# Optimization experiments

Hardware: AMD Instinct MI355X
Metric: run time of the kernel (lower is better)

## Reference

```python
import jax, jax.numpy as jnp
import numpy as np

B, L, H, F, K, NBINS, T = 32, 512, 512, 512, 3, 256, 4096
EPS = 1e-8  # RMSNorm epsilon
PAD = (K - 1) // 2  # =1, matches both conv paddings in the torch module


def _conv1d(x, w, b):
    # x: [B, L, Cin], w: [K, Cin, Cout]
    return jax.lax.conv_general_dilated(
        x, w, window_strides=(1,), padding=[(PAD, PAD)],
        dimension_numbers=('NLC', 'LIO', 'NLC')) + b


def _rms(x, g):
    return g * x / (jnp.sqrt(jnp.mean(x * x, axis=-1, keepdims=True)) + EPS)


def _vpred(x, mask, w1, b1, g1, w2, b2, g2, wl, bl):
    h = _rms(jax.nn.relu(_conv1d(x, w1, b1)), g1)
    h = _rms(jax.nn.relu(_conv1d(h, w2, b2)), g2)
    out = (h @ wl + bl)[..., 0]  # [B, L]
    return jnp.where(mask, 0.0, out)


def _proj(x, w1, b1, w2, b2):
    return jax.nn.relu(jax.nn.relu(x @ w1 + b1) @ w2 + b2)


def _length_regulate(x, dur, max_len):
    # Vectorized equivalent of LengthRegulator: repeat phoneme i dur[b,i] times, pad to max_len.
    cum = jnp.cumsum(dur, axis=1)               # [B, L]
    mel_len = cum[:, -1]                        # [B]
    t = jnp.arange(max_len)                     # [T]
    idx = jax.vmap(lambda c: jnp.searchsorted(c, t, side='right'))(cum)  # [B, T]
    idx = jnp.minimum(idx, x.shape[1] - 1)
    out = jnp.take_along_axis(x, idx[:, :, None], axis=1)  # [B, T, H]
    valid = (t[None, :] < mel_len[:, None])
    return out * valid[:, :, None].astype(x.dtype), mel_len


def setup_inputs() -> dict:
    key = jax.random.key(0)
    ks = iter(jax.random.split(key, 64))
    n = lambda *s: jax.random.normal(next(ks), s, jnp.float32) * 0.05
    inp = {}
    inp['x'] = jax.random.normal(next(ks), (B, L, H), jnp.float32)
    inp['embedding'] = jax.random.normal(next(ks), (B, L, H), jnp.float32)
    inp['src_mask'] = jnp.zeros((B, L), bool)
    inp['duration_target'] = jax.random.randint(next(ks), (B, L), 0, 9, jnp.int32)
    inp['pitch_target'] = jax.random.normal(next(ks), (B, L), jnp.float32)
    inp['energy_target'] = jax.random.normal(next(ks), (B, L), jnp.float32)
    inp['max_len'] = T
    for p in ['dur', 'pit', 'eng']:
        inp[p + '_w1'] = n(K, H, F); inp[p + '_b1'] = jnp.zeros(F, jnp.float32)
        inp[p + '_g1'] = jnp.ones(F, jnp.float32)
        inp[p + '_w2'] = n(K, F, F); inp[p + '_b2'] = jnp.zeros(F, jnp.float32)
        inp[p + '_g2'] = jnp.ones(F, jnp.float32)
        inp[p + '_wl'] = n(F, 1); inp[p + '_bl'] = jnp.zeros(1, jnp.float32)
    for p in ['pp', 'ep', 'sp']:
        inp[p + '_w1'] = n(H, H); inp[p + '_b1'] = jnp.zeros(H, jnp.float32)
        inp[p + '_w2'] = n(H, H); inp[p + '_b2'] = jnp.zeros(H, jnp.float32)
    inp['pitch_bins'] = jnp.linspace(-3.0, 3.0, NBINS - 1)
    inp['energy_bins'] = jnp.linspace(-3.0, 3.0, NBINS - 1)
    inp['pitch_emb'] = n(NBINS, H)
    inp['energy_emb'] = n(NBINS, H)
    return inp


def reference(x, embedding, src_mask, duration_target, pitch_target, energy_target, max_len,
              dur_w1, dur_b1, dur_g1, dur_w2, dur_b2, dur_g2, dur_wl, dur_bl,
              pit_w1, pit_b1, pit_g1, pit_w2, pit_b2, pit_g2, pit_wl, pit_bl,
              eng_w1, eng_b1, eng_g1, eng_w2, eng_b2, eng_g2, eng_wl, eng_bl,
              pp_w1, pp_b1, pp_w2, pp_b2,
              ep_w1, ep_b1, ep_w2, ep_b2,
              sp_w1, sp_b1, sp_w2, sp_b2,
              pitch_bins, energy_bins, pitch_emb, energy_emb):
    log_dur = _vpred(x, src_mask, dur_w1, dur_b1, dur_g1, dur_w2, dur_b2, dur_g2, dur_wl, dur_bl)
    pit_pred = _vpred(x + _proj(embedding, pp_w1, pp_b1, pp_w2, pp_b2), src_mask,
                      pit_w1, pit_b1, pit_g1, pit_w2, pit_b2, pit_g2, pit_wl, pit_bl)
    pitch_embedding = pitch_emb[jnp.searchsorted(pitch_bins, pitch_target)]  # torch.bucketize right=False == side='left'
    eng_pred = _vpred(x + _proj(embedding, ep_w1, ep_b1, ep_w2, ep_b2), src_mask,
                      eng_w1, eng_b1, eng_g1, eng_w2, eng_b2, eng_g2, eng_wl, eng_bl)
    energy_embedding = energy_emb[jnp.searchsorted(energy_bins, energy_target)]
    xo = x + energy_embedding + pitch_embedding + _proj(embedding, sp_w1, sp_b1, sp_w2, sp_b2)
    out, mel_len = _length_regulate(xo, duration_target, max_len)
    return (out, pit_pred, eng_pred, log_dur, mel_len)
```

## Files before the change

### kernel.cpp

```cpp
#include <hip/hip_runtime.h>

#define Bv    32
#define Lv    512
#define Hv    512
#define Fv    512
#define Tv    4096
#define Mv    (Bv*Lv)
#define NBINSv 256

#define OUT_OFF 0
#define PIT_OFF (Bv*(size_t)Tv*Hv)
#define ENG_OFF (PIT_OFF + Mv)
#define DUR_OFF (ENG_OFF + Mv)
#define MEL_OFF (DUR_OFF + Mv)

typedef unsigned short ushort;
typedef __attribute__((ext_vector_type(8))) short   bf16x8;
typedef __attribute__((ext_vector_type(4))) float   f32x4;
typedef __attribute__((ext_vector_type(8))) unsigned short u16x8;

__device__ __forceinline__ float b2f(ushort u) {
    union { float f; unsigned u; } x; x.u = ((unsigned)u) << 16; return x.f;
}
__device__ __forceinline__ ushort f2b(float f) {
    union { float f; unsigned u; } x; x.f = f;
    unsigned r = x.u + 0x7fffu + ((x.u >> 16) & 1u);
    return (ushort)(r >> 16);
}

#define GLL16(g, l) __builtin_amdgcn_global_load_lds( \
    (const __attribute__((address_space(1))) void*)(g), \
    (__attribute__((address_space(3))) void*)(l), 16, 0, 0)

template<int NTAPS, int EPI>
__global__ __launch_bounds__(256) void gemm_bf16_kernel(
    const ushort* __restrict__ A, const ushort* __restrict__ Bt,
    const float* __restrict__ bias, ushort* __restrict__ C,
    const float* __restrict__ res, const float* __restrict__ pe,
    const float* __restrict__ ee, const int* __restrict__ idxp,
    const int* __restrict__ idxe, const ushort* __restrict__ zp)
{
    constexpr int KTOT = NTAPS * 512;
    __shared__ ushort As[128 * 32];
    __shared__ ushort Bs[128 * 32];

    const int tid = threadIdx.x;
    const int n0 = blockIdx.x * 128;
    const int m0 = blockIdx.y * 128;

    const int sar = tid >> 2;
    const int sl  = tid & 3;

    const int lane = tid & 63;
    const int w    = tid >> 6;
    const int wm   = (w & 1) * 64;
    const int wn   = (w >> 1) * 64;
    const int lr   = lane & 15;
    const int q    = lane >> 4;

    f32x4 acc[4][4];
    #pragma unroll
    for (int i = 0; i < 4; ++i)
        #pragma unroll
        for (int j = 0; j < 4; ++j) {
            f32x4 z = {0.f, 0.f, 0.f, 0.f};
            acc[i][j] = z;
        }

    for (int kt = 0; kt < NTAPS * 16; ++kt) {
        const int tap = (NTAPS == 3) ? (kt >> 4) : 0;
        const int kin = (NTAPS == 3) ? ((kt & 15) << 5) : (kt << 5);

        #pragma unroll
        for (int r = 0; r < 2; ++r) {
            const int row = sar + r * 64;
            const int m   = m0 + row;
            const int qg  = (sl - (row >> 1)) & 3;
            const ushort* asrc;
            if (NTAPS == 3) {
                const int l  = m & (Lv - 1);
                const int ls = l + tap - 1;
                asrc = ((unsigned)ls < (unsigned)Lv)
                     ? A + (size_t)(m + tap - 1) * 512 + kin + qg * 8
                     : zp;
            } else {
                asrc = A + (size_t)m * 512 + kin + qg * 8;
            }
            GLL16(asrc, &As[row * 32 + sl * 8]);
            const ushort* bsrc = Bt + (size_t)(n0 + row) * KTOT + tap * 512 + kin + qg * 8;
            GLL16(bsrc, &Bs[row * 32 + sl * 8]);
        }
        __syncthreads();

        bf16x8 af[4], bf[4];
        #pragma unroll
        for (int i = 0; i < 4; ++i) {
            const int rm = wm + i * 16 + lr;
            af[i] = *(const bf16x8*)&As[rm * 32 + (((q + (rm >> 1)) & 3) << 3)];
            const int rn = wn + i * 16 + lr;
            bf[i] = *(const bf16x8*)&Bs[rn * 32 + (((q + (rn >> 1)) & 3) << 3)];
        }
        #pragma unroll
        for (int i = 0; i < 4; ++i)
            #pragma unroll
            for (int j = 0; j < 4; ++j)
                acc[i][j] = __builtin_amdgcn_mfma_f32_16x16x32_bf16(
                                af[i], bf[j], acc[i][j], 0, 0, 0);
        __syncthreads();
    }

    #pragma unroll
    for (int i = 0; i < 4; ++i) {
        #pragma unroll
        for (int r = 0; r < 4; ++r) {
            const int m = m0 + wm + i * 16 + q * 4 + r;
            const size_t ro = (size_t)m * 512;
            int ip = 0, ie = 0;
            if (EPI == 2) { ip = idxp[m]; ie = idxe[m]; }
            #pragma unroll
            for (int j = 0; j < 4; ++j) {
                const int n = n0 + wn + j * 16 + lr;
                float v = acc[i][j][r] + bias[n];
                v = fmaxf(v, 0.f);
                if (EPI >= 1) v += res[ro + n];
                if (EPI == 2) v += pe[(size_t)ip * 512 + n] + ee[(size_t)ie * 512 + n];
                C[ro + n] = f2b(v);
            }
        }
    }
}

__global__ __launch_bounds__(256) void convert_kernel(
    const float* __restrict__ X, ushort* __restrict__ Xb)
{
    const size_t i = (size_t)blockIdx.x * 256 + threadIdx.x;
    const float4 a = ((const float4*)X)[2 * i];
    const float4 b = ((const float4*)X)[2 * i + 1];
    u16x8 o;
    o[0] = f2b(a.x); o[1] = f2b(a.y); o[2] = f2b(a.z); o[3] = f2b(a.w);
    o[4] = f2b(b.x); o[5] = f2b(b.y); o[6] = f2b(b.z); o[7] = f2b(b.w);
    *(u16x8*)(Xb + i * 8) = o;
}

__global__ __launch_bounds__(256) void transpose_kernel(
    const float* __restrict__ W, ushort* __restrict__ Wt, int Ktot)
{
    __shared__ float t[32][33];
    const int k0 = blockIdx.x * 32, n0 = blockIdx.y * 32;
    const int r = threadIdx.x >> 5, c = threadIdx.x & 31;
    #pragma unroll
    for (int rr = 0; rr < 4; ++rr)
        t[r + rr * 8][c] = W[(size_t)(k0 + r + rr * 8) * 512 + n0 + c];
    __syncthreads();
    #pragma unroll
    for (int rr = 0; rr < 4; ++rr)
        Wt[(size_t)(n0 + r + rr * 8) * Ktot + k0 + c] = f2b(t[c][r + rr * 8]);
}

__global__ __launch_bounds__(128) void rms_kernel(
    const ushort* __restrict__ h, const float* __restrict__ g, ushort* __restrict__ o)
{
    const int row = blockIdx.x;
    const int tid = threadIdx.x;
    const ushort4 hv = ((const ushort4*)(h + (size_t)row * 512))[tid];
    const float v0 = b2f(hv.x), v1 = b2f(hv.y), v2 = b2f(hv.z), v3 = b2f(hv.w);
    float ss = v0 * v0 + v1 * v1 + v2 * v2 + v3 * v3;
    #pragma unroll
    for (int off = 32; off; off >>= 1) ss += __shfl_down(ss, off, 64);
    __shared__ float p[2];
    if ((tid & 63) == 0) p[tid >> 6] = ss;
    __syncthreads();
    const float tot = p[0] + p[1];
    const float inv = 1.f / (sqrtf(tot * (1.f / 512.f)) + 1e-8f);
    const float4 gv = ((const float4*)g)[tid];
    ushort4 ov;
    ov.x = f2b(gv.x * v0 * inv); ov.y = f2b(gv.y * v1 * inv);
    ov.z = f2b(gv.z * v2 * inv); ov.w = f2b(gv.w * v3 * inv);
    ((ushort4*)(o + (size_t)row * 512))[tid] = ov;
}

__global__ __launch_bounds__(256) void linear_kernel(
    const ushort* __restrict__ h, const float* __restrict__ wl,
    const float* __restrict__ bl, const unsigned char* __restrict__ mask,
    float* __restrict__ o)
{
    const int wave = threadIdx.x >> 6, lane = threadIdx.x & 63;
    const int row = blockIdx.x * 4 + wave;
    const bf16x8 hv = *(const bf16x8*)(h + (size_t)row * 512 + lane * 8);
    float s = 0.f;
    #pragma unroll
    for (int t = 0; t < 8; ++t) s += b2f((ushort)hv[t]) * wl[lane * 8 + t];
    #pragma unroll
    for (int off = 32; off; off >>= 1) s += __shfl_down(s, off, 64);
    if (lane == 0) o[row] = mask[row] ? 0.f : (s + bl[0]);
}

__global__ __launch_bounds__(256) void idx_kernel(
    const float* __restrict__ pt, const float* __restrict__ et,
    const float* __restrict__ pbins, const float* __restrict__ ebins,
    int* __restrict__ idxp, int* __restrict__ idxe)
{
    __shared__ float pb[NBINSv - 1], eb[NBINSv - 1];
    const int tid = threadIdx.x;
    if (tid < NBINSv - 1) { pb[tid] = pbins[tid]; eb[tid] = ebins[tid]; }
    __syncthreads();
    const int m = blockIdx.x * 256 + tid;
    const float pv = pt[m], ev = et[m];
    int lo = 0, hi = NBINSv - 1;
    while (lo < hi) { int mid = (lo + hi) >> 1; if (pb[mid] < pv) lo = mid + 1; else hi = mid; }
    idxp[m] = lo;
    lo = 0; hi = NBINSv - 1;
    while (lo < hi) { int mid = (lo + hi) >> 1; if (eb[mid] < ev) lo = mid + 1; else hi = mid; }
    idxe[m] = lo;
}

__global__ __launch_bounds__(512) void cumsum_kernel(
    const int* __restrict__ dur, int* __restrict__ cum,
    int* __restrict__ melint, float* __restrict__ melout)
{
    __shared__ int s[Lv];
    const int b = blockIdx.x, tid = threadIdx.x;
    s[tid] = dur[b * Lv + tid];
    __syncthreads();
    for (int off = 1; off < Lv; off <<= 1) {
        int t = (tid >= off) ? s[tid - off] : 0;
        __syncthreads();
        s[tid] += t;
        __syncthreads();
    }
    cum[b * Lv + tid] = s[tid];
    if (tid == Lv - 1) { melint[b] = s[tid]; melout[b] = (float)s[tid]; }
}

__global__ __launch_bounds__(128) void regulate_kernel(
    const ushort* __restrict__ xo, const int* __restrict__ cum,
    const int* __restrict__ melint, float* __restrict__ out)
{
    const int bt = blockIdx.x;
    const int b = bt >> 12;
    const int t = bt & (Tv - 1);
    const int* c = cum + b * Lv;
    int lo = 0, hi = Lv;
    while (lo < hi) { int mid = (lo + hi) >> 1; if (c[mid] <= t) lo = mid + 1; else hi = mid; }
    const int idx = min(lo, Lv - 1);
    float4 v = make_float4(0.f, 0.f, 0.f, 0.f);
    if (t < melint[b]) {
        const ushort4 u = ((const ushort4*)(xo + (size_t)(b * Lv + idx) * 512))[threadIdx.x];
        v.x = b2f(u.x); v.y = b2f(u.y); v.z = b2f(u.z); v.w = b2f(u.w);
    }
    ((float4*)(out + (size_t)bt * 512))[threadIdx.x] = v;
}

extern "C" void kernel_launch(void* const* d_in, const int* in_sizes, int n_in,
                              void* d_out, int out_size, void* d_ws, size_t ws_size,
                              hipStream_t stream)
{
    const float* x    = (const float*)d_in[0];
    const float* emb  = (const float*)d_in[1];
    const unsigned char* mask = (const unsigned char*)d_in[2];
    const int*   durt = (const int*)d_in[3];
    const float* pt   = (const float*)d_in[4];
    const float* et   = (const float*)d_in[5];
    const float* dw1 = (const float*)d_in[7],  *db1 = (const float*)d_in[8],
               * dg1 = (const float*)d_in[9],  *dw2 = (const float*)d_in[10],
               * db2 = (const float*)d_in[11], *dg2 = (const float*)d_in[12],
               * dwl = (const float*)d_in[13], *dbl = (const float*)d_in[14];
    const float* pw1 = (const float*)d_in[15], *pb1 = (const float*)d_in[16],
               * pg1 = (const float*)d_in[17], *pw2 = (const float*)d_in[18],
               * pb2 = (const float*)d_in[19], *pg2 = (const float*)d_in[20],
               * pwl = (const float*)d_in[21], *pbl = (const float*)d_in[22];
    const float* ew1 = (const float*)d_in[23], *eb1 = (const float*)d_in[24],
               * eg1 = (const float*)d_in[25], *ew2 = (const float*)d_in[26],
               * eb2 = (const float*)d_in[27], *eg2 = (const float*)d_in[28],
               * ewl = (const float*)d_in[29], *ebl = (const float*)d_in[30];
    const float* ppw1 = (const float*)d_in[31], *ppb1 = (const float*)d_in[32],
               * ppw2 = (const float*)d_in[33], *ppb2 = (const float*)d_in[34];
    const float* epw1 = (const float*)d_in[35], *epb1 = (const float*)d_in[36],
               * epw2 = (const float*)d_in[37], *epb2 = (const float*)d_in[38];
    const float* spw1 = (const float*)d_in[39], *spb1 = (const float*)d_in[40],
               * spw2 = (const float*)d_in[41], *spb2 = (const float*)d_in[42];
    const float* pbins = (const float*)d_in[43];
    const float* ebins = (const float*)d_in[44];
    const float* pemb  = (const float*)d_in[45];
    const float* eemb  = (const float*)d_in[46];

    float* outf = (float*)d_out;

    int*    cum    = (int*)d_ws;
    int*    melint = cum + Mv;
    int*    idxp   = melint + 64;
    int*    idxe   = idxp + Mv;
    ushort* zp     = (ushort*)((float*)d_ws + 49216);
    ushort* xob    = (ushort*)((float*)d_ws + 65536);

    ushort* xb   = (ushort*)(outf + 0);
    ushort* eb   = (ushort*)(outf + 4194304);
    ushort* bufA = (ushort*)(outf + 8388608);
    ushort* bufC = (ushort*)(outf + 12582912);
    ushort* bufD = (ushort*)(outf + 16777216);
    ushort* wt[12];
    {
        size_t off = 20971520;
        for (int i = 0; i < 6; ++i) { wt[i] = (ushort*)(outf + off); off += 393216; }
        for (int i = 6; i < 12; ++i) { wt[i] = (ushort*)(outf + off); off += 131072; }
    }

    hipMemsetAsync(zp, 0, 64, stream);

    convert_kernel<<<4096, 256, 0, stream>>>(x, xb);
    convert_kernel<<<4096, 256, 0, stream>>>(emb, eb);
    const dim3 tg3(48, 16), tg1(16, 16);
    transpose_kernel<<<tg3, 256, 0, stream>>>(dw1, wt[0], 1536);
    transpose_kernel<<<tg3, 256, 0, stream>>>(dw2, wt[1], 1536);
    transpose_kernel<<<tg3, 256, 0, stream>>>(pw1, wt[2], 1536);
    transpose_kernel<<<tg3, 256, 0, stream>>>(pw2, wt[3], 1536);
    transpose_kernel<<<tg3, 256, 0, stream>>>(ew1, wt[4], 1536);
    transpose_kernel<<<tg3, 256, 0, stream>>>(ew2, wt[5], 1536);
    transpose_kernel<<<tg1, 256, 0, stream>>>(ppw1, wt[6],  512);
    transpose_kernel<<<tg1, 256, 0, stream>>>(ppw2, wt[7],  512);
    transpose_kernel<<<tg1, 256, 0, stream>>>(epw1, wt[8],  512);
    transpose_kernel<<<tg1, 256, 0, stream>>>(epw2, wt[9],  512);
    transpose_kernel<<<tg1, 256, 0, stream>>>(spw1, wt[10], 512);
    transpose_kernel<<<tg1, 256, 0, stream>>>(spw2, wt[11], 512);

    idx_kernel<<<Mv / 256, 256, 0, stream>>>(pt, et, pbins, ebins, idxp, idxe);
    cumsum_kernel<<<Bv, Lv, 0, stream>>>(durt, cum, melint, outf + MEL_OFF);

    const dim3 ggrid(Fv / 128, Mv / 128);

    auto vpred = [&](const ushort* xin, const ushort* w1t, const float* b1, const float* g1,
                     const ushort* w2t, const float* b2, const float* g2,
                     const float* wl, const float* bl, float* pred) {
        gemm_bf16_kernel<3, 0><<<ggrid, 256, 0, stream>>>(xin, w1t, b1, bufC,
            nullptr, nullptr, nullptr, nullptr, nullptr, zp);
        rms_kernel<<<Mv, 128, 0, stream>>>(bufC, g1, bufD);
        gemm_bf16_kernel<3, 0><<<ggrid, 256, 0, stream>>>(bufD, w2t, b2, bufC,
            nullptr, nullptr, nullptr, nullptr, nullptr, zp);
        rms_kernel<<<Mv, 128, 0, stream>>>(bufC, g2, bufD);
        linear_kernel<<<Mv / 4, 256, 0, stream>>>(bufD, wl, bl, mask, pred);
    };

    vpred(xb, wt[0], db1, dg1, wt[1], db2, dg2, dwl, dbl, outf + DUR_OFF);

    gemm_bf16_kernel<1, 0><<<ggrid, 256, 0, stream>>>(eb, wt[6], ppb1, bufA,
        nullptr, nullptr, nullptr, nullptr, nullptr, zp);
    gemm_bf16_kernel<1, 1><<<ggrid, 256, 0, stream>>>(bufA, wt[7], ppb2, xob,
        x, nullptr, nullptr, nullptr, nullptr, zp);
    vpred(xob, wt[2], pb1, pg1, wt[3], pb2, pg2, pwl, pbl, outf + PIT_OFF);

    gemm_bf16_kernel<1, 0><<<ggrid, 256, 0, stream>>>(eb, wt[8], epb1, bufA,
        nullptr, nullptr, nullptr, nullptr, nullptr, zp);
    gemm_bf16_kernel<1, 1><<<ggrid, 256, 0, stream>>>(bufA, wt[9], epb2, xob,
        x, nullptr, nullptr, nullptr, nullptr, zp);
    vpred(xob, wt[4], eb1, eg1, wt[5], eb2, eg2, ewl, ebl, outf + ENG_OFF);

    gemm_bf16_kernel<1, 0><<<ggrid, 256, 0, stream>>>(eb, wt[10], spb1, bufA,
        nullptr, nullptr, nullptr, nullptr, nullptr, zp);
    gemm_bf16_kernel<1, 2><<<ggrid, 256, 0, stream>>>(bufA, wt[11], spb2, xob,
        x, pemb, eemb, idxp, idxe, zp);

    regulate_kernel<<<Bv * Tv, 128, 0, stream>>>(xob, cum, melint, outf + OUT_OFF);
}
```

Measured before the change: 916.4 us.

## Batch the three predictor branches into grid-z launches and fuse final RMSNorm into linear

The pitch, energy and duration predictors now run together: each GEMM and RMSNorm stage is one launch, with blockIdx.z selecting the branch through pointer-array argument structs. The converts and transposes are batched the same way. The second RMSNorm is folded into the output projection, which computes the sum of squares and the g·w dot product in one pass and skips writing the normalized tensor. The length-regulator index search moves into a separate per-frame tmap kernel. The aim is fewer launches and more blocks per GEMM (a 4x128x3 grid) to fill the GPU, at the cost of separate intermediate buffers for each branch and a larger memory footprint.

New measurement: 844.9 us. 1.08x faster.

```diff
diff --git a/kernel.cpp b/kernel.cpp
--- a/kernel.cpp
+++ b/kernel.cpp
@@ -32,15 +32,30 @@
     (const __attribute__((address_space(1))) void*)(g), \
     (__attribute__((address_space(3))) void*)(l), 16, 0, 0)
 
-template<int NTAPS, int EPI>
+template<int NZ> struct GArgs {
+    const ushort* A[NZ];
+    const ushort* W[NZ];
+    const float*  bias[NZ];
+    ushort*       C[NZ];
+};
+struct RmsArgs   { const ushort* h[3]; const float* g[3]; ushort* o[3]; };
+struct RlArgs    { const ushort* h[3]; const float* g[3]; const float* wl[3]; const float* bl[3]; };
+struct TransArgs { const float* src[6]; ushort* dst[6]; };
+struct ConvArgs  { const float* src[2]; ushort* dst[2]; };
+
+template<int NTAPS, int EPI, int NZ>
 __global__ __launch_bounds__(256) void gemm_bf16_kernel(
-    const ushort* __restrict__ A, const ushort* __restrict__ Bt,
-    const float* __restrict__ bias, ushort* __restrict__ C,
-    const float* __restrict__ res, const float* __restrict__ pe,
+    GArgs<NZ> ga, const float* __restrict__ res, const float* __restrict__ pe,
     const float* __restrict__ ee, const int* __restrict__ idxp,
     const int* __restrict__ idxe, const ushort* __restrict__ zp)
 {
     constexpr int KTOT = NTAPS * 512;
+    const int z = (NZ > 1) ? blockIdx.z : 0;
+    const ushort* __restrict__ A    = ga.A[z];
+    const ushort* __restrict__ Bt   = ga.W[z];
+    const float*  __restrict__ bias = ga.bias[z];
+    ushort*       __restrict__ C    = ga.C[z];
+
     __shared__ ushort As[128 * 32];
     __shared__ ushort Bs[128 * 32];
 
@@ -63,8 +78,8 @@
     for (int i = 0; i < 4; ++i)
         #pragma unroll
         for (int j = 0; j < 4; ++j) {
-            f32x4 z = {0.f, 0.f, 0.f, 0.f};
-            acc[i][j] = z;
+            f32x4 zz = {0.f, 0.f, 0.f, 0.f};
+            acc[i][j] = zz;
         }
 
     for (int kt = 0; kt < NTAPS * 16; ++kt) {
@@ -92,20 +107,20 @@
         }
         __syncthreads();
 
-        bf16x8 af[4], bf[4];
+        bf16x8 af[4], bfr[4];
         #pragma unroll
         for (int i = 0; i < 4; ++i) {
             const int rm = wm + i * 16 + lr;
-            af[i] = *(const bf16x8*)&As[rm * 32 + (((q + (rm >> 1)) & 3) << 3)];
+            af[i]  = *(const bf16x8*)&As[rm * 32 + (((q + (rm >> 1)) & 3) << 3)];
             const int rn = wn + i * 16 + lr;
-            bf[i] = *(const bf16x8*)&Bs[rn * 32 + (((q + (rn >> 1)) & 3) << 3)];
+            bfr[i] = *(const bf16x8*)&Bs[rn * 32 + (((q + (rn >> 1)) & 3) << 3)];
         }
         #pragma unroll
         for (int i = 0; i < 4; ++i)
             #pragma unroll
             for (int j = 0; j < 4; ++j)
                 acc[i][j] = __builtin_amdgcn_mfma_f32_16x16x32_bf16(
-                                af[i], bf[j], acc[i][j], 0, 0, 0);
+                                af[i], bfr[j], acc[i][j], 0, 0, 0);
         __syncthreads();
     }
 
@@ -130,9 +145,10 @@
     }
 }
 
-__global__ __launch_bounds__(256) void convert_kernel(
-    const float* __restrict__ X, ushort* __restrict__ Xb)
-{
+__global__ __launch_bounds__(256) void convert_kernel(ConvArgs ca)
+{
+    const float* __restrict__ X  = ca.src[blockIdx.y];
+    ushort*      __restrict__ Xb = ca.dst[blockIdx.y];
     const size_t i = (size_t)blockIdx.x * 256 + threadIdx.x;
     const float4 a = ((const float4*)X)[2 * i];
     const float4 b = ((const float4*)X)[2 * i + 1];
@@ -142,9 +158,10 @@
     *(u16x8*)(Xb + i * 8) = o;
 }
 
-__global__ __launch_bounds__(256) void transpose_kernel(
-    const float* __restrict__ W, ushort* __restrict__ Wt, int Ktot)
-{
+__global__ __launch_bounds__(256) void transpose_kernel(TransArgs ta, int Ktot)
+{
+    const float* __restrict__ W  = ta.src[blockIdx.z];
+    ushort*      __restrict__ Wt = ta.dst[blockIdx.z];
     __shared__ float t[32][33];
     const int k0 = blockIdx.x * 32, n0 = blockIdx.y * 32;
     const int r = threadIdx.x >> 5, c = threadIdx.x & 31;
@@ -157,11 +174,12 @@
         Wt[(size_t)(n0 + r + rr * 8) * Ktot + k0 + c] = f2b(t[c][r + rr * 8]);
 }
 
-__global__ __launch_bounds__(128) void rms_kernel(
-    const ushort* __restrict__ h, const float* __restrict__ g, ushort* __restrict__ o)
-{
+__global__ __launch_bounds__(128) void rms_kernel(RmsArgs ra)
+{
+    const int z = blockIdx.y;
     const int row = blockIdx.x;
     const int tid = threadIdx.x;
+    const ushort* __restrict__ h = ra.h[z];
     const ushort4 hv = ((const ushort4*)(h + (size_t)row * 512))[tid];
     const float v0 = b2f(hv.x), v1 = b2f(hv.y), v2 = b2f(hv.z), v3 = b2f(hv.w);
     float ss = v0 * v0 + v1 * v1 + v2 * v2 + v3 * v3;
@@ -172,27 +190,42 @@
     __syncthreads();
     const float tot = p[0] + p[1];
     const float inv = 1.f / (sqrtf(tot * (1.f / 512.f)) + 1e-8f);
-    const float4 gv = ((const float4*)g)[tid];
+    const float4 gv = ((const float4*)ra.g[z])[tid];
     ushort4 ov;
     ov.x = f2b(gv.x * v0 * inv); ov.y = f2b(gv.y * v1 * inv);
     ov.z = f2b(gv.z * v2 * inv); ov.w = f2b(gv.w * v3 * inv);
-    ((ushort4*)(o + (size_t)row * 512))[tid] = ov;
-}
-
-__global__ __launch_bounds__(256) void linear_kernel(
-    const ushort* __restrict__ h, const float* __restrict__ wl,
-    const float* __restrict__ bl, const unsigned char* __restrict__ mask,
-    float* __restrict__ o)
-{
+    ((ushort4*)(ra.o[z] + (size_t)row * 512))[tid] = ov;
+}
+
+__global__ __launch_bounds__(256) void rmslin_kernel(
+    RlArgs ra, const unsigned char* __restrict__ mask, float* __restrict__ predbase)
+{
+    const int z = blockIdx.y;
     const int wave = threadIdx.x >> 6, lane = threadIdx.x & 63;
     const int row = blockIdx.x * 4 + wave;
+    const ushort* __restrict__ h = ra.h[z];
     const bf16x8 hv = *(const bf16x8*)(h + (size_t)row * 512 + lane * 8);
-    float s = 0.f;
-    #pragma unroll
-    for (int t = 0; t < 8; ++t) s += b2f((ushort)hv[t]) * wl[lane * 8 + t];
-    #pragma unroll
-    for (int off = 32; off; off >>= 1) s += __shfl_down(s, off, 64);
-    if (lane == 0) o[row] = mask[row] ? 0.f : (s + bl[0]);
+    const float4 g0 = *(const float4*)(ra.g[z] + lane * 8);
+    const float4 g1 = *(const float4*)(ra.g[z] + lane * 8 + 4);
+    const float4 w0 = *(const float4*)(ra.wl[z] + lane * 8);
+    const float4 w1 = *(const float4*)(ra.wl[z] + lane * 8 + 4);
+    float hf[8];
+    #pragma unroll
+    for (int t = 0; t < 8; ++t) hf[t] = b2f((ushort)hv[t]);
+    float ss = 0.f, sgw = 0.f;
+    #pragma unroll
+    for (int t = 0; t < 8; ++t) ss += hf[t] * hf[t];
+    sgw += hf[0]*g0.x*w0.x + hf[1]*g0.y*w0.y + hf[2]*g0.z*w0.z + hf[3]*g0.w*w0.w;
+    sgw += hf[4]*g1.x*w1.x + hf[5]*g1.y*w1.y + hf[6]*g1.z*w1.z + hf[7]*g1.w*w1.w;
+    #pragma unroll
+    for (int off = 32; off; off >>= 1) {
+        ss  += __shfl_down(ss,  off, 64);
+        sgw += __shfl_down(sgw, off, 64);
+    }
+    if (lane == 0) {
+        const float inv = 1.f / (sqrtf(ss * (1.f / 512.f)) + 1e-8f);
+        predbase[(size_t)z * Mv + row] = mask[row] ? 0.f : (sgw * inv + ra.bl[z][0]);
+    }
 }
 
 __global__ __launch_bounds__(256) void idx_kernel(
@@ -200,9 +233,9 @@
     const float* __restrict__ pbins, const float* __restrict__ ebins,
     int* __restrict__ idxp, int* __restrict__ idxe)
 {
-    __shared__ float pb[NBINSv - 1], eb[NBINSv - 1];
+    __shared__ float pb[NBINSv - 1], ebn[NBINSv - 1];
     const int tid = threadIdx.x;
-    if (tid < NBINSv - 1) { pb[tid] = pbins[tid]; eb[tid] = ebins[tid]; }
+    if (tid < NBINSv - 1) { pb[tid] = pbins[tid]; ebn[tid] = ebins[tid]; }
     __syncthreads();
     const int m = blockIdx.x * 256 + tid;
     const float pv = pt[m], ev = et[m];
@@ -210,7 +243,7 @@
     while (lo < hi) { int mid = (lo + hi) >> 1; if (pb[mid] < pv) lo = mid + 1; else hi = mid; }
     idxp[m] = lo;
     lo = 0; hi = NBINSv - 1;
-    while (lo < hi) { int mid = (lo + hi) >> 1; if (eb[mid] < ev) lo = mid + 1; else hi = mid; }
+    while (lo < hi) { int mid = (lo + hi) >> 1; if (ebn[mid] < ev) lo = mid + 1; else hi = mid; }
     idxe[m] = lo;
 }
 
@@ -232,20 +265,28 @@
     if (tid == Lv - 1) { melint[b] = s[tid]; melout[b] = (float)s[tid]; }
 }
 
-__global__ __launch_bounds__(128) void regulate_kernel(
-    const ushort* __restrict__ xo, const int* __restrict__ cum,
-    const int* __restrict__ melint, float* __restrict__ out)
-{
-    const int bt = blockIdx.x;
+__global__ __launch_bounds__(256) void tmap_kernel(
+    const int* __restrict__ cum, const int* __restrict__ melint,
+    int* __restrict__ tmap)
+{
+    const int bt = blockIdx.x * 256 + threadIdx.x;
     const int b = bt >> 12;
     const int t = bt & (Tv - 1);
     const int* c = cum + b * Lv;
     int lo = 0, hi = Lv;
     while (lo < hi) { int mid = (lo + hi) >> 1; if (c[mid] <= t) lo = mid + 1; else hi = mid; }
-    const int idx = min(lo, Lv - 1);
+    tmap[bt] = (t < melint[b]) ? (b * Lv + min(lo, Lv - 1)) : -1;
+}
+
+__global__ __launch_bounds__(128) void regulate_kernel(
+    const ushort* __restrict__ xo, const int* __restrict__ tmap,
+    float* __restrict__ out)
+{
+    const int bt = blockIdx.x;
+    const int src = tmap[bt];
     float4 v = make_float4(0.f, 0.f, 0.f, 0.f);
-    if (t < melint[b]) {
-        const ushort4 u = ((const ushort4*)(xo + (size_t)(b * Lv + idx) * 512))[threadIdx.x];
+    if (src >= 0) {
+        const ushort4 u = ((const ushort4*)(xo + (size_t)src * 512))[threadIdx.x];
         v.x = b2f(u.x); v.y = b2f(u.y); v.z = b2f(u.z); v.w = b2f(u.w);
     }
     ((float4*)(out + (size_t)bt * 512))[threadIdx.x] = v;
@@ -287,77 +328,63 @@
     float* outf = (float*)d_out;
 
     int*    cum    = (int*)d_ws;
-    int*    melint = cum + Mv;
+    int*    melint = cum + 16384;
     int*    idxp   = melint + 64;
-    int*    idxe   = idxp + Mv;
-    ushort* zp     = (ushort*)((float*)d_ws + 49216);
-    ushort* xob    = (ushort*)((float*)d_ws + 65536);
-
-    ushort* xb   = (ushort*)(outf + 0);
-    ushort* eb   = (ushort*)(outf + 4194304);
-    ushort* bufA = (ushort*)(outf + 8388608);
-    ushort* bufC = (ushort*)(outf + 12582912);
-    ushort* bufD = (ushort*)(outf + 16777216);
+    int*    idxe   = idxp + 16384;
+    ushort* zp     = (ushort*)(idxe + 16384);
+    int*    tmap   = idxe + 16448;
+    ushort* xob    = (ushort*)((float*)d_ws + 262144);
+
+    #define OBUF(i) ((ushort*)(outf + (size_t)(i) * 4194304))
+    ushort* xb  = OBUF(0);   ushort* eb  = OBUF(1);
+    ushort* pA0 = OBUF(2);   ushort* pA1 = OBUF(3);  ushort* pA2 = OBUF(4);
+    ushort* xp  = OBUF(5);   ushort* xe  = OBUF(6);
+    ushort* c0  = OBUF(7);   ushort* c1  = OBUF(8);  ushort* c2  = OBUF(9);
+    ushort* r0  = OBUF(10);  ushort* r1  = OBUF(11); ushort* r2  = OBUF(12);
     ushort* wt[12];
     {
-        size_t off = 20971520;
-        for (int i = 0; i < 6; ++i) { wt[i] = (ushort*)(outf + off); off += 393216; }
+        size_t off = 13ull * 4194304;
+        for (int i = 0; i < 6; ++i)  { wt[i] = (ushort*)(outf + off); off += 393216; }
         for (int i = 6; i < 12; ++i) { wt[i] = (ushort*)(outf + off); off += 131072; }
     }
 
     hipMemsetAsync(zp, 0, 64, stream);
 
-    convert_kernel<<<4096, 256, 0, stream>>>(x, xb);
-    convert_kernel<<<4096, 256, 0, stream>>>(emb, eb);
-    const dim3 tg3(48, 16), tg1(16, 16);
-    transpose_kernel<<<tg3, 256, 0, stream>>>(dw1, wt[0], 1536);
-    transpose_kernel<<<tg3, 256, 0, stream>>>(dw2, wt[1], 1536);
-    transpose_kernel<<<tg3, 256, 0, stream>>>(pw1, wt[2], 1536);
-    transpose_kernel<<<tg3, 256, 0, stream>>>(pw2, wt[3], 1536);
-    transpose_kernel<<<tg3, 256, 0, stream>>>(ew1, wt[4], 1536);
-    transpose_kernel<<<tg3, 256, 0, stream>>>(ew2, wt[5], 1536);
-    transpose_kernel<<<tg1, 256, 0, stream>>>(ppw1, wt[6],  512);
-    transpose_kernel<<<tg1, 256, 0, stream>>>(ppw2, wt[7],  512);
-    transpose_kernel<<<tg1, 256, 0, stream>>>(epw1, wt[8],  512);
-    transpose_kernel<<<tg1, 256, 0, stream>>>(epw2, wt[9],  512);
-    transpose_kernel<<<tg1, 256, 0, stream>>>(spw1, wt[10], 512);
-    transpose_kernel<<<tg1, 256, 0, stream>>>(spw2, wt[11], 512);
+    { ConvArgs ca = {{x, emb}, {xb, eb}};
+      convert_kernel<<<dim3(4096, 2), 256, 0, stream>>>(ca); }
+    { TransArgs ta = {{dw1, dw2, pw1, pw2, ew1, ew2}, {wt[0], wt[1], wt[2], wt[3], wt[4], wt[5]}};
+      transpose_kernel<<<dim3(48, 16, 6), 256, 0, stream>>>(ta, 1536); }
+    { TransArgs ta = {{ppw1, ppw2, epw1, epw2, spw1, spw2},
+                      {wt[6], wt[7], wt[8], wt[9], wt[10], wt[11]}};
+      transpose_kernel<<<dim3(16, 16, 6), 256, 0, stream>>>(ta, 512); }
 
     idx_kernel<<<Mv / 256, 256, 0, stream>>>(pt, et, pbins, ebins, idxp, idxe);
     cumsum_kernel<<<Bv, Lv, 0, stream>>>(durt, cum, melint, outf + MEL_OFF);
-
-    const dim3 ggrid(Fv / 128, Mv / 128);
-
-    auto vpred = [&](const ushort* xin, const ushort* w1t, const float* b1, const float* g1,
-                     const ushort* w2t, const float* b2, const float* g2,
-                     const float* wl, const float* bl, float* pred) {
-        gemm_bf16_kernel<3, 0><<<ggrid, 256, 0, stream>>>(xin, w1t, b1, bufC,
-            nullptr, nullptr, nullptr, nullptr, nullptr, zp);
-        rms_kernel<<<Mv, 128, 0, stream>>>(bufC, g1, bufD);
-        gemm_bf16_kernel<3, 0><<<ggrid, 256, 0, stream>>>(bufD, w2t, b2, bufC,
-            nullptr, nullptr, nullptr, nullptr, nullptr, zp);
-        rms_kernel<<<Mv, 128, 0, stream>>>(bufC, g2, bufD);
-        linear_kernel<<<Mv / 4, 256, 0, stream>>>(bufD, wl, bl, mask, pred);
-    };
-
-    vpred(xb, wt[0], db1, dg1, wt[1], db2, dg2, dwl, dbl, outf + DUR_OFF);
-
-    gemm_bf16_kernel<1, 0><<<ggrid, 256, 0, stream>>>(eb, wt[6], ppb1, bufA,
-        nullptr, nullptr, nullptr, nullptr, nullptr, zp);
-    gemm_bf16_kernel<1, 1><<<ggrid, 256, 0, stream>>>(bufA, wt[7], ppb2, xob,
-        x, nullptr, nullptr, nullptr, nullptr, zp);
-    vpred(xob, wt[2], pb1, pg1, wt[3], pb2, pg2, pwl, pbl, outf + PIT_OFF);
-
-    gemm_bf16_kernel<1, 0><<<ggrid, 256, 0, stream>>>(eb, wt[8], epb1, bufA,
-        nullptr, nullptr, nullptr, nullptr, nullptr, zp);
-    gemm_bf16_kernel<1, 1><<<ggrid, 256, 0, stream>>>(bufA, wt[9], epb2, xob,
-        x, nullptr, nullptr, nullptr, nullptr, zp);
-    vpred(xob, wt[4], eb1, eg1, wt[5], eb2, eg2, ewl, ebl, outf + ENG_OFF);
-
-    gemm_bf16_kernel<1, 0><<<ggrid, 256, 0, stream>>>(eb, wt[10], spb1, bufA,
-        nullptr, nullptr, nullptr, nullptr, nullptr, zp);
-    gemm_bf16_kernel<1, 2><<<ggrid, 256, 0, stream>>>(bufA, wt[11], spb2, xob,
-        x, pemb, eemb, idxp, idxe, zp);
-
-    regulate_kernel<<<Bv * Tv, 128, 0, stream>>>(xob, cum, melint, outf + OUT_OFF);
-}
+    tmap_kernel<<<Bv * Tv / 256, 256, 0, stream>>>(cum, melint, tmap);
+
+    const dim3 g3(Fv / 128, Mv / 128, 3);
+    const dim3 g2(Fv / 128, Mv / 128, 2);
+    const dim3 g1(Fv / 128, Mv / 128, 1);
+
+    { GArgs<3> a = {{eb, eb, eb}, {wt[6], wt[8], wt[10]}, {ppb1, epb1, spb1}, {pA0, pA1, pA2}};
+      gemm_bf16_kernel<1, 0, 3><<<g3, 256, 0, stream>>>(a, nullptr, nullptr, nullptr,
+                                                        nullptr, nullptr, zp); }
+    { GArgs<2> a = {{pA0, pA1}, {wt[7], wt[9]}, {ppb2, epb2}, {xp, xe}};
+      gemm_bf16_kernel<1, 1, 2><<<g2, 256, 0, stream>>>(a, x, nullptr, nullptr,
+                                                        nullptr, nullptr, zp); }
+    { GArgs<1> a = {{pA2}, {wt[11]}, {spb2}, {xob}};
+      gemm_bf16_kernel<1, 2, 1><<<g1, 256, 0, stream>>>(a, x, pemb, eemb, idxp, idxe, zp); }
+
+    { GArgs<3> a = {{xp, xe, xb}, {wt[2], wt[4], wt[0]}, {pb1, eb1, db1}, {c0, c1, c2}};
+      gemm_bf16_kernel<3, 0, 3><<<g3, 256, 0, stream>>>(a, nullptr, nullptr, nullptr,
+                                                        nullptr, nullptr, zp); }
+    { RmsArgs ra = {{c0, c1, c2}, {pg1, eg1, dg1}, {r0, r1, r2}};
+      rms_kernel<<<dim3(Mv, 3), 128, 0, stream>>>(ra); }
+    { GArgs<3> a = {{r0, r1, r2}, {wt[3], wt[5], wt[1]}, {pb2, eb2, db2}, {c0, c1, c2}};
+      gemm_bf16_kernel<3, 0, 3><<<g3, 256, 0, stream>>>(a, nullptr, nullptr, nullptr,
+                                                        nullptr, nullptr, zp); }
+    { RlArgs ra = {{c0, c1, c2}, {pg2, eg2, dg2}, {pwl, ewl, dwl}, {pbl, ebl, dbl}};
+      rmslin_kernel<<<dim3(Mv / 4, 3), 256, 0, stream>>>(ra, mask, outf + PIT_OFF); }
+
+    regulate_kernel<<<Bv * Tv, 128, 0, stream>>>(xob, tmap, outf + OUT_OFF);
+}
```
